# Optimization experiments

Hardware: AMD Instinct MI355X
Metric: run time of the kernel (lower is better)

The kernel has to match this reference:

```python
import jax, jax.numpy as jnp
import numpy as np
from jax import lax

B, T, H, E, V, ENC = 2048, 48, 512, 256, 128, 1024


def setup_inputs() -> dict:
    key = jax.random.key(0)
    ks = jax.random.split(key, 13)
    s = 0.05  # weight scale to keep activations sane
    return {
        "tgt_ids": jax.random.randint(ks[0], (B, T), 0, V),
        "enc_hid": jax.random.normal(ks[1], (B, ENC), jnp.float32),
        "W_init1": s * jax.random.normal(ks[2], (ENC, H), jnp.float32),
        "W_init2": s * jax.random.normal(ks[3], (ENC, H), jnp.float32),
        "embed_table": s * jax.random.normal(ks[4], (V, E), jnp.float32),
        "k1": s * jax.random.normal(ks[5], (E, 3 * H), jnp.float32),
        "rk1": s * jax.random.normal(ks[6], (H, 3 * H), jnp.float32),
        "b1": jnp.zeros((2, 3 * H), jnp.float32),
        "k2": s * jax.random.normal(ks[7], (H, 3 * H), jnp.float32),
        "rk2": s * jax.random.normal(ks[8], (H, 3 * H), jnp.float32),
        "b2": jnp.zeros((2, 3 * H), jnp.float32),
        "Wv": s * jax.random.normal(ks[9], (H, V), jnp.float32),
        "bv": jnp.zeros((V,), jnp.float32),
    }


def gru_masked(x_proj, mask, h0, rk, rb):
    """Keras GRU (reset_after=True, gate order z,r,h) with mask carry-through.
    x_proj: [B,T,3H] precomputed x@kernel + input_bias. mask: [B,T] bool.
    Masked steps keep previous state AND previous output (Keras masking semantics;
    GRU output == state)."""
    def step(h, inp):
        xg, m = inp  # xg: [B,3H], m: [B]
        inner = h @ rk + rb  # [B,3H]
        xz, xr, xh = jnp.split(xg, 3, axis=-1)
        rz, rr, rh = jnp.split(inner, 3, axis=-1)
        z = jax.nn.sigmoid(xz + rz)
        r = jax.nn.sigmoid(xr + rr)
        hh = jnp.tanh(xh + r * rh)
        h_new = z * h + (1.0 - z) * hh
        h = jnp.where(m[:, None], h_new, h)
        return h, h

    _, seq = lax.scan(step, h0, (x_proj.transpose(1, 0, 2), mask.T))
    return seq.transpose(1, 0, 2)  # [B,T,H]


def reference(tgt_ids, enc_hid, W_init1, W_init2, embed_table,
              k1, rk1, b1, k2, rk2, b2, Wv, bv):
    mask = tgt_ids != 0  # mask_zero=True
    emb = embed_table[tgt_ids]  # [B,T,E]
    h01 = enc_hid @ W_init1  # Dense no-bias init of layer-1 state
    h02 = enc_hid @ W_init2
    x1 = emb @ k1 + b1[0]  # [B,T,3H]
    seq1 = gru_masked(x1, mask, h01, rk1, b1[1])
    x2 = seq1 @ k2 + b2[0]
    seq2 = gru_masked(x2, mask, h02, rk2, b2[1])
    probs = jax.nn.softmax(seq2 @ Wv + bv, axis=-1)  # [B,T,V]
    return probs
```

## Files before the change

kernel.cpp:

```cpp
#include <hip/hip_runtime.h>
#include <hip/hip_bf16.h>
#include <math.h>

#define B_   2048
#define T_   48
#define H_   512
#define E_   256
#define V_   128
#define ENC_ 1024
#define H3_  1536
#define BH_  (B_ * H_)
#define NBLK_ 512

typedef __attribute__((ext_vector_type(8))) short bf16x8;
typedef __attribute__((ext_vector_type(4))) float f32x4;
typedef unsigned short ushort_t;

#if defined(__has_builtin)
#if __has_builtin(__builtin_amdgcn_global_load_lds)
#define HAVE_ASYNC 1
#endif
#endif
#ifndef HAVE_ASYNC
#define HAVE_ASYNC 0
#endif

__device__ __forceinline__ void stage16(const ushort_t* g, ushort_t* l, int lane)
{
#if HAVE_ASYNC
    __builtin_amdgcn_global_load_lds(
        (const __attribute__((address_space(1))) unsigned int*)g,
        (__attribute__((address_space(3))) unsigned int*)l, 16, 0, 0);
#else
    *(bf16x8*)(l + lane * 8) = *(const bf16x8*)g;
#endif
}

__device__ __forceinline__ float sigmoidf_(float x) { return 1.0f / (1.0f + expf(-x)); }

__device__ __forceinline__ void tile_map(int lin, int& m0, int& i0)
{
    i0 = ((((lin & 7) << 1) | ((lin >> 3) & 1))) * 32;
    m0 = (lin >> 4) * 64;
}

constexpr int BM = 64, BN = 64, BK = 16;

__global__ __launch_bounds__(256) void gemm_f32(
    const float* __restrict__ A, const float* __restrict__ Bm,
    const float* __restrict__ bias, float* __restrict__ C,
    int M, int N, int K)
{
    __shared__ float As[BK][BM + 4];
    __shared__ float Bs[BK][BN + 4];

    const int tid = threadIdx.x;
    const int bm = blockIdx.y * BM;
    const int bn = blockIdx.x * BN;
    const int tm = (tid >> 4) * 4;
    const int tn = (tid & 15) * 4;
    const int lmA = tid >> 2;
    const int lkA = (tid & 3) * 4;
    const int lkB = tid >> 4;
    const int lnB = (tid & 15) * 4;

    float acc[4][4] = {};

    for (int k0 = 0; k0 < K; k0 += BK) {
        float4 av  = *(const float4*)(A  + (size_t)(bm + lmA) * K + (k0 + lkA));
        float4 bv4 = *(const float4*)(Bm + (size_t)(k0 + lkB) * N + (bn + lnB));
        As[lkA + 0][lmA] = av.x;
        As[lkA + 1][lmA] = av.y;
        As[lkA + 2][lmA] = av.z;
        As[lkA + 3][lmA] = av.w;
        *(float4*)&Bs[lkB][lnB] = bv4;
        __syncthreads();

        #pragma unroll
        for (int k = 0; k < BK; ++k) {
            float4 a = *(const float4*)&As[k][tm];
            float4 b = *(const float4*)&Bs[k][tn];
            acc[0][0] += a.x * b.x; acc[0][1] += a.x * b.y; acc[0][2] += a.x * b.z; acc[0][3] += a.x * b.w;
            acc[1][0] += a.y * b.x; acc[1][1] += a.y * b.y; acc[1][2] += a.y * b.z; acc[1][3] += a.y * b.w;
            acc[2][0] += a.z * b.x; acc[2][1] += a.z * b.y; acc[2][2] += a.z * b.z; acc[2][3] += a.z * b.w;
            acc[3][0] += a.w * b.x; acc[3][1] += a.w * b.y; acc[3][2] += a.w * b.z; acc[3][3] += a.w * b.w;
        }
        __syncthreads();
    }

    #pragma unroll
    for (int r = 0; r < 4; ++r)
        #pragma unroll
        for (int c = 0; c < 4; ++c) {
            float v = acc[r][c];
            if (bias) v += bias[bn + tn + c];
            C[(size_t)(bm + tm + r) * N + (bn + tn + c)] = v;
        }
}

__global__ __launch_bounds__(256) void transpose_to_bf16(
    const float* __restrict__ W, __hip_bfloat16* __restrict__ Wt, int K, int N)
{
    __shared__ float tile[32][33];
    const int bk = blockIdx.y * 32, bn = blockIdx.x * 32;
    const int tx = threadIdx.x & 31, ty = threadIdx.x >> 5;
    #pragma unroll
    for (int i = ty; i < 32; i += 8)
        tile[i][tx] = W[(size_t)(bk + i) * N + (bn + tx)];
    __syncthreads();
    #pragma unroll
    for (int i = ty; i < 32; i += 8)
        Wt[(size_t)(bn + i) * K + (bk + tx)] = __float2bfloat16(tile[tx][i]);
}

__global__ __launch_bounds__(256) void transpose_split(
    const float* __restrict__ W, __hip_bfloat16* __restrict__ Whi,
    __hip_bfloat16* __restrict__ Wlo, int K, int N)
{
    __shared__ float tile[32][33];
    const int bk = blockIdx.y * 32, bn = blockIdx.x * 32;
    const int tx = threadIdx.x & 31, ty = threadIdx.x >> 5;
    #pragma unroll
    for (int i = ty; i < 32; i += 8)
        tile[i][tx] = W[(size_t)(bk + i) * N + (bn + tx)];
    __syncthreads();
    #pragma unroll
    for (int i = ty; i < 32; i += 8) {
        const float v = tile[tx][i];
        const __hip_bfloat16 h = __float2bfloat16(v);
        Whi[(size_t)(bn + i) * K + (bk + tx)] = h;
        Wlo[(size_t)(bn + i) * K + (bk + tx)] = __float2bfloat16(v - __bfloat162float(h));
    }
}

__global__ __launch_bounds__(256) void split_cast(
    const float* __restrict__ x, __hip_bfloat16* __restrict__ hi,
    __hip_bfloat16* __restrict__ lo, int n)
{
    const int i0 = (blockIdx.x * 256 + threadIdx.x) * 4;
    if (i0 >= n) return;
    const float4 v = *(const float4*)(x + i0);
    const float vv[4] = { v.x, v.y, v.z, v.w };
    #pragma unroll
    for (int j = 0; j < 4; ++j) {
        const __hip_bfloat16 h = __float2bfloat16(vv[j]);
        hi[i0 + j] = h;
        lo[i0 + j] = __float2bfloat16(vv[j] - __bfloat162float(h));
    }
}

__global__ __launch_bounds__(256, 2) void init_mfma(
    const ushort_t* __restrict__ ehi, const ushort_t* __restrict__ elo,
    const ushort_t* __restrict__ w1hi, const ushort_t* __restrict__ w1lo,
    const ushort_t* __restrict__ w2hi, const ushort_t* __restrict__ w2lo,
    float* __restrict__ h1f, __hip_bfloat16* __restrict__ h1b,
    float* __restrict__ h2f, __hip_bfloat16* __restrict__ h2b)
{
    const ushort_t* whi = blockIdx.z ? w2hi : w1hi;
    const ushort_t* wlo = blockIdx.z ? w2lo : w1lo;
    float* hf = blockIdx.z ? h2f : h1f;
    __hip_bfloat16* hb = blockIdx.z ? h2b : h1b;

    __shared__ __attribute__((aligned(16))) ushort_t Ahi[2][4096];
    __shared__ __attribute__((aligned(16))) ushort_t Alo[2][4096];
    __shared__ __attribute__((aligned(16))) ushort_t Bhi[2][2048];
    __shared__ __attribute__((aligned(16))) ushort_t Blo[2][2048];

    const int tid  = threadIdx.x;
    const int lane = tid & 63;
    const int w    = tid >> 6;
    const int ln   = lane & 15;
    const int kg   = lane >> 4;
    const int wr   = w >> 1, wc = w & 1;
    const int m0   = blockIdx.y * 64;
    const int i0   = blockIdx.x * 32;

    const int crow = lane >> 3;
    const int ckof = ((lane & 7) ^ crow) * 8;
    const int ko0 = (kg * 8) ^ ((ln & 7) * 8);
    const int ko1 = (32 + kg * 8) ^ ((ln & 7) * 8);

    auto STG = [&](int pb, int k0) {
        #pragma unroll
        for (int c = w; c < 24; c += 4) {
            const ushort_t* g; ushort_t* l;
            if (c < 8) {
                g = ehi + (size_t)(m0 + c * 8 + crow) * ENC_ + k0 + ckof;
                l = &Ahi[pb][c * 512];
            } else if (c < 16) {
                const int cc = c - 8;
                g = elo + (size_t)(m0 + cc * 8 + crow) * ENC_ + k0 + ckof;
                l = &Alo[pb][cc * 512];
            } else if (c < 20) {
                const int cc = c - 16;
                g = whi + (size_t)(i0 + cc * 8 + crow) * ENC_ + k0 + ckof;
                l = &Bhi[pb][cc * 512];
            } else {
                const int cc = c - 20;
                g = wlo + (size_t)(i0 + cc * 8 + crow) * ENC_ + k0 + ckof;
                l = &Blo[pb][cc * 512];
            }
            stage16(g, l, lane);
        }
    };

    f32x4 acc[2] = {};
    STG(0, 0);
    __syncthreads();
    int buf = 0;
    for (int k0 = 0; k0 < ENC_; k0 += 64) {
        if (k0 + 64 < ENC_) STG(buf ^ 1, k0 + 64);
        #pragma unroll
        for (int kk = 0; kk < 2; ++kk) {
            const int ko = kk ? ko1 : ko0;
            bf16x8 ah[2], al[2], bh, bl;
            #pragma unroll
            for (int fm = 0; fm < 2; ++fm) {
                ah[fm] = *(const bf16x8*)(&Ahi[buf][(wr * 32 + fm * 16 + ln) * 64 + ko]);
                al[fm] = *(const bf16x8*)(&Alo[buf][(wr * 32 + fm * 16 + ln) * 64 + ko]);
            }
            bh = *(const bf16x8*)(&Bhi[buf][(wc * 16 + ln) * 64 + ko]);
            bl = *(const bf16x8*)(&Blo[buf][(wc * 16 + ln) * 64 + ko]);
            #pragma unroll
            for (int fm = 0; fm < 2; ++fm) {
                acc[fm] = __builtin_amdgcn_mfma_f32_16x16x32_bf16(ah[fm], bh, acc[fm], 0, 0, 0);
                acc[fm] = __builtin_amdgcn_mfma_f32_16x16x32_bf16(al[fm], bh, acc[fm], 0, 0, 0);
                acc[fm] = __builtin_amdgcn_mfma_f32_16x16x32_bf16(ah[fm], bl, acc[fm], 0, 0, 0);
            }
        }
        __syncthreads();
        buf ^= 1;
    }

    const int i = i0 + wc * 16 + ln;
    #pragma unroll
    for (int fm = 0; fm < 2; ++fm)
        #pragma unroll
        for (int r = 0; r < 4; ++r) {
            const int b = m0 + wr * 32 + fm * 16 + kg * 4 + r;
            const float v = acc[fm][r];
            hf[(size_t)b * H_ + i] = v;
            hb[(size_t)b * H_ + i] = __float2bfloat16(v);
        }
}

__device__ __forceinline__ void l1_phase(
    ushort_t* Al0, ushort_t* Bl0,
    int m0, int i0, int i, int t,
    const int* __restrict__ tgt, const float* __restrict__ xe1,
    const ushort_t* __restrict__ rkt,
    float rbz, float rbr, float rbh,
    const ushort_t* __restrict__ hb_cur,
    __hip_bfloat16* __restrict__ hb_nxt,
    float (&hv)[2][4])
{
    const int tid  = threadIdx.x;
    const int lane = tid & 63;
    const int w    = tid >> 6;
    const int ln   = lane & 15;
    const int kg   = lane >> 4;
    const int wr   = w >> 1, wc = w & 1;
    (void)wc;

    const int crow = lane >> 3;
    const int ckof = ((lane & 7) ^ crow) * 8;

    int ids[2][4];
    #pragma unroll
    for (int fm = 0; fm < 2; ++fm)
        #pragma unroll
        for (int r = 0; r < 4; ++r) {
            const int b = m0 + wr * 32 + fm * 16 + kg * 4 + r;
            ids[fm][r] = tgt[(size_t)b * T_ + t];
        }
    float xgz[2][4], xgr[2][4], xgh[2][4];
    #pragma unroll
    for (int fm = 0; fm < 2; ++fm)
        #pragma unroll
        for (int r = 0; r < 4; ++r) {
            const float* xg = xe1 + (size_t)ids[fm][r] * H3_;
            xgz[fm][r] = xg[i]; xgr[fm][r] = xg[H_ + i]; xgh[fm][r] = xg[2 * H_ + i];
        }

    const int ko0 = (kg * 8) ^ ((ln & 7) * 8);
    const int ko1 = (32 + kg * 8) ^ ((ln & 7) * 8);

    f32x4 acc[2][3] = {};

    auto STAGE = [&](int pb, int k0) {
        #pragma unroll
        for (int c = w; c < 20; c += 4) {
            const ushort_t* g; ushort_t* l;
            if (c < 8) {
                g = hb_cur + (size_t)(m0 + c * 8 + crow) * H_ + k0 + ckof;
                l = Al0 + pb * 4096 + c * 512;
            } else {
                const int idx = c - 8;
                g = rkt + (size_t)((idx >> 2) * H_ + i0 + (idx & 3) * 8 + crow) * H_ + k0 + ckof;
                l = Bl0 + pb * 6144 + idx * 512;
            }
            stage16(g, l, lane);
        }
    };

    STAGE(0, 0);
    __syncthreads();
    int buf = 0;
    for (int k0 = 0; k0 < H_; k0 += 64) {
        if (k0 + 64 < H_) STAGE(buf ^ 1, k0 + 64);
        #pragma unroll
        for (int kk = 0; kk < 2; ++kk) {
            const int ko = kk ? ko1 : ko0;
            bf16x8 af[2], bf[3];
            #pragma unroll
            for (int fm = 0; fm < 2; ++fm)
                af[fm] = *(const bf16x8*)(Al0 + buf * 4096 + (wr * 32 + fm * 16 + ln) * 64 + ko);
            #pragma unroll
            for (int g = 0; g < 3; ++g)
                bf[g] = *(const bf16x8*)(Bl0 + buf * 6144 + g * 2048 + ((w & 1) * 16 + ln) * 64 + ko);
            #pragma unroll
            for (int fm = 0; fm < 2; ++fm)
                #pragma unroll
                for (int g = 0; g < 3; ++g)
                    acc[fm][g] = __builtin_amdgcn_mfma_f32_16x16x32_bf16(
                        af[fm], bf[g], acc[fm][g], 0, 0, 0);
        }
        __syncthreads();
        buf ^= 1;
    }

    #pragma unroll
    for (int fm = 0; fm < 2; ++fm)
        #pragma unroll
        for (int r = 0; r < 4; ++r) {
            const int b = m0 + wr * 32 + fm * 16 + kg * 4 + r;
            const float hvv = hv[fm][r];
            float z  = sigmoidf_(xgz[fm][r] + acc[fm][0][r] + rbz);
            float rr = sigmoidf_(xgr[fm][r] + acc[fm][1][r] + rbr);
            float hh = tanhf(xgh[fm][r] + rr * (acc[fm][2][r] + rbh));
            float hn = (ids[fm][r] != 0) ? (z * hvv + (1.0f - z) * hh) : hvv;
            hv[fm][r] = hn;
            hb_nxt[(size_t)b * H_ + i] = __float2bfloat16(hn);
        }
}

__device__ __forceinline__ void l2_phase(
    ushort_t* lds,
    int m0, int i0, int i, int t,
    const int* __restrict__ tgt,
    const ushort_t* __restrict__ k2t, const ushort_t* __restrict__ rk2t,
    float bxz, float bxr, float bxh,
    float brz, float brr, float brh,
    const ushort_t* __restrict__ s1b,
    const ushort_t* __restrict__ a1, size_t a1s,
    __hip_bfloat16* __restrict__ hbo, size_t hos,
    float (&hv)[2][4])
{
    ushort_t* A0l = lds;
    ushort_t* A1l = lds + 8192;
    ushort_t* B0l = lds + 16384;
    ushort_t* B1l = lds + 22528;

    const int tid  = threadIdx.x;
    const int lane = tid & 63;
    const int w    = tid >> 6;
    const int ln   = lane & 15;
    const int kg   = lane >> 4;
    const int wr   = w >> 1, wc = w & 1;
    (void)wc;

    const int crow = lane >> 3;
    const int ckof = ((lane & 7) ^ crow) * 8;

    int ids[2][4];
    #pragma unroll
    for (int fm = 0; fm < 2; ++fm)
        #pragma unroll
        for (int r = 0; r < 4; ++r) {
            const int b = m0 + wr * 32 + fm * 16 + kg * 4 + r;
            ids[fm][r] = tgt[(size_t)b * T_ + t];
        }

    const int ko0 = (kg * 8) ^ ((ln & 7) * 8);
    const int ko1 = (32 + kg * 8) ^ ((ln & 7) * 8);

    auto STAGE_A = [&](int pb, int k0) {
        #pragma unroll
        for (int c = w; c < 16; c += 4) {
            const ushort_t* g; ushort_t* l;
            if (c < 8) {
                g = s1b + (size_t)(m0 + c * 8 + crow) * H_ + k0 + ckof;
                l = A0l + pb * 4096 + c * 512;
            } else {
                const int cc = c - 8;
                g = a1 + (size_t)(m0 + cc * 8 + crow) * a1s + k0 + ckof;
                l = A1l + pb * 4096 + cc * 512;
            }
            stage16(g, l, lane);
        }
    };
    auto STAGE_B = [&](int k0) {
        #pragma unroll
        for (int c = w; c < 24; c += 4) {
            const ushort_t* g; ushort_t* l;
            if (c < 12) {
                g = k2t + (size_t)((c >> 2) * H_ + i0 + (c & 3) * 8 + crow) * H_ + k0 + ckof;
                l = B0l + c * 512;
            } else {
                const int idx = c - 12;
                g = rk2t + (size_t)((idx >> 2) * H_ + i0 + (idx & 3) * 8 + crow) * H_ + k0 + ckof;
                l = B1l + idx * 512;
            }
            stage16(g, l, lane);
        }
    };

    f32x4 acc0[2][3] = {};
    f32x4 acc1[2][3] = {};

    STAGE_A(0, 0);
    STAGE_B(0);
    __syncthreads();
    int buf = 0;
    for (int k0 = 0; k0 < H_; k0 += 64) {
        const bool more = (k0 + 64 < H_);
        if (more) STAGE_A(buf ^ 1, k0 + 64);

        bf16x8 a0f[2][2], a1f[2][2], b0f[2][3], b1f[2][3];
        #pragma unroll
        for (int kk = 0; kk < 2; ++kk) {
            const int ko = kk ? ko1 : ko0;
            #pragma unroll
            for (int fm = 0; fm < 2; ++fm) {
                a0f[kk][fm] = *(const bf16x8*)(A0l + buf * 4096 + (wr * 32 + fm * 16 + ln) * 64 + ko);
                a1f[kk][fm] = *(const bf16x8*)(A1l + buf * 4096 + (wr * 32 + fm * 16 + ln) * 64 + ko);
            }
            #pragma unroll
            for (int g = 0; g < 3; ++g) {
                b0f[kk][g] = *(const bf16x8*)(B0l + g * 2048 + ((w & 1) * 16 + ln) * 64 + ko);
                b1f[kk][g] = *(const bf16x8*)(B1l + g * 2048 + ((w & 1) * 16 + ln) * 64 + ko);
            }
        }
        __builtin_amdgcn_sched_barrier(0);
        asm volatile("s_waitcnt lgkmcnt(0)" ::: "memory");
        __builtin_amdgcn_sched_barrier(0);
        __builtin_amdgcn_s_barrier();
        if (more) STAGE_B(k0 + 64);

        #pragma unroll
        for (int kk = 0; kk < 2; ++kk)
            #pragma unroll
            for (int fm = 0; fm < 2; ++fm)
                #pragma unroll
                for (int g = 0; g < 3; ++g) {
                    acc0[fm][g] = __builtin_amdgcn_mfma_f32_16x16x32_bf16(
                        a0f[kk][fm], b0f[kk][g], acc0[fm][g], 0, 0, 0);
                    acc1[fm][g] = __builtin_amdgcn_mfma_f32_16x16x32_bf16(
                        a1f[kk][fm], b1f[kk][g], acc1[fm][g], 0, 0, 0);
                }
        __syncthreads();
        buf ^= 1;
    }

    #pragma unroll
    for (int fm = 0; fm < 2; ++fm)
        #pragma unroll
        for (int r = 0; r < 4; ++r) {
            const int b = m0 + wr * 32 + fm * 16 + kg * 4 + r;
            const float hvv = hv[fm][r];
            float z  = sigmoidf_((acc0[fm][0][r] + bxz) + (acc1[fm][0][r] + brz));
            float rr = sigmoidf_((acc0[fm][1][r] + bxr) + (acc1[fm][1][r] + brr));
            float hh = tanhf((acc0[fm][2][r] + bxh) + rr * (acc1[fm][2][r] + brh));
            float hn = (ids[fm][r] != 0) ? (z * hvv + (1.0f - z) * hh) : hvv;
            hv[fm][r] = hn;
            hbo[(size_t)b * hos + i] = __float2bfloat16(hn);
        }
}

__global__ __launch_bounds__(256, 2) void l1_fused(
    const int* __restrict__ tgt, int t,
    const float* __restrict__ xe1, const ushort_t* __restrict__ rkt,
    const float* __restrict__ rb,
    const float* __restrict__ hf_cur, const ushort_t* __restrict__ hb_cur,
    float* __restrict__ hf_nxt, __hip_bfloat16* __restrict__ hb_nxt)
{
    __shared__ __attribute__((aligned(16))) ushort_t lds[20480];
    int m0, i0; tile_map(blockIdx.x, m0, i0);
    const int tid = threadIdx.x, lane = tid & 63, w = tid >> 6;
    const int ln = lane & 15, kg = lane >> 4, wr = w >> 1, wc = w & 1;
    const int i = i0 + wc * 16 + ln;

    float hv[2][4];
    #pragma unroll
    for (int fm = 0; fm < 2; ++fm)
        #pragma unroll
        for (int r = 0; r < 4; ++r)
            hv[fm][r] = hf_cur[(size_t)(m0 + wr * 32 + fm * 16 + kg * 4 + r) * H_ + i];

    l1_phase(lds, lds + 8192, m0, i0, i, t, tgt, xe1, rkt,
             rb[i], rb[H_ + i], rb[2 * H_ + i], hb_cur, hb_nxt, hv);

    #pragma unroll
    for (int fm = 0; fm < 2; ++fm)
        #pragma unroll
        for (int r = 0; r < 4; ++r)
            hf_nxt[(size_t)(m0 + wr * 32 + fm * 16 + kg * 4 + r) * H_ + i] = hv[fm][r];
}

__global__ __launch_bounds__(256, 2) void l2_fused(
    const int* __restrict__ tgt, int t,
    const ushort_t* __restrict__ k2t, const ushort_t* __restrict__ rk2t,
    const float* __restrict__ bx, const float* __restrict__ br,
    const ushort_t* __restrict__ s1b,
    const float* __restrict__ hf_cur,
    const ushort_t* __restrict__ hb_cur, size_t hbs,
    float* __restrict__ hf_nxt,
    __hip_bfloat16* __restrict__ hbo, size_t hos)
{
    __shared__ __attribute__((aligned(16))) ushort_t lds[28672];
    int m0, i0; tile_map(blockIdx.x, m0, i0);
    const int tid = threadIdx.x, lane = tid & 63, w = tid >> 6;
    const int ln = lane & 15, kg = lane >> 4, wr = w >> 1, wc = w & 1;
    const int i = i0 + wc * 16 + ln;

    float hv[2][4];
    #pragma unroll
    for (int fm = 0; fm < 2; ++fm)
        #pragma unroll
        for (int r = 0; r < 4; ++r)
            hv[fm][r] = hf_cur[(size_t)(m0 + wr * 32 + fm * 16 + kg * 4 + r) * H_ + i];

    l2_phase(lds, m0, i0, i, t, tgt, k2t, rk2t,
             bx[i], bx[H_ + i], bx[2 * H_ + i],
             br[i], br[H_ + i], br[2 * H_ + i],
             s1b, hb_cur, hbs, hbo, hos, hv);

    #pragma unroll
    for (int fm = 0; fm < 2; ++fm)
        #pragma unroll
        for (int r = 0; r < 4; ++r)
            hf_nxt[(size_t)(m0 + wr * 32 + fm * 16 + kg * 4 + r) * H_ + i] = hv[fm][r];
}

__device__ __forceinline__ void grid_barrier(unsigned* bar)
{
    __syncthreads();
    if (threadIdx.x == 0) {
        __threadfence();
        const unsigned g = __hip_atomic_load(&bar[1], __ATOMIC_RELAXED, __HIP_MEMORY_SCOPE_AGENT);
        const unsigned arrived =
            __hip_atomic_fetch_add(&bar[0], 1u, __ATOMIC_ACQ_REL, __HIP_MEMORY_SCOPE_AGENT) + 1u;
        if (arrived == (unsigned)NBLK_) {
            __hip_atomic_store(&bar[0], 0u, __ATOMIC_RELAXED, __HIP_MEMORY_SCOPE_AGENT);
            __hip_atomic_store(&bar[1], g + 1u, __ATOMIC_RELEASE, __HIP_MEMORY_SCOPE_AGENT);
        } else {
            while (__hip_atomic_load(&bar[1], __ATOMIC_ACQUIRE, __HIP_MEMORY_SCOPE_AGENT) == g)
                __builtin_amdgcn_s_sleep(2);
        }
        __threadfence();
    }
    __syncthreads();
}

__global__ __launch_bounds__(256, 2) void recurrence_all(
    const int* __restrict__ tgt, const float* __restrict__ xe1,
    const ushort_t* __restrict__ rk1t, const float* __restrict__ rb1,
    const ushort_t* __restrict__ k2t, const ushort_t* __restrict__ rk2t,
    const float* __restrict__ bx, const float* __restrict__ br,
    const float* __restrict__ h1f0, __hip_bfloat16* __restrict__ h1b,
    const float* __restrict__ h2f0, const __hip_bfloat16* __restrict__ h2b0,
    __hip_bfloat16* __restrict__ seq2b, unsigned* __restrict__ bar)
{
    __shared__ __attribute__((aligned(16))) ushort_t lds[28672];
    int m0, i0; tile_map(blockIdx.x, m0, i0);
    const int tid = threadIdx.x, lane = tid & 63, w = tid >> 6;
    const int ln = lane & 15, kg = lane >> 4, wr = w >> 1, wc = w & 1;
    const int i = i0 + wc * 16 + ln;

    const float rbz = rb1[i], rbr = rb1[H_ + i], rbh = rb1[2 * H_ + i];
    const float bxz = bx[i],  bxr = bx[H_ + i],  bxh = bx[2 * H_ + i];
    const float brz = br[i],  brr = br[H_ + i],  brh = br[2 * H_ + i];

    float hv1[2][4], hv2[2][4];
    #pragma unroll
    for (int fm = 0; fm < 2; ++fm)
        #pragma unroll
        for (int r = 0; r < 4; ++r) {
            const size_t b = (size_t)(m0 + wr * 32 + fm * 16 + kg * 4 + r) * H_ + i;
            hv1[fm][r] = h1f0[b];
            hv2[fm][r] = h2f0[b];
        }

    l1_phase(lds, lds + 8192, m0, i0, i, 0, tgt, xe1, rk1t, rbz, rbr, rbh,
             (const ushort_t*)h1b, h1b + BH_, hv1);
    grid_barrier(bar);

    #pragma unroll 1
    for (int p = 0; p < T_; ++p) {
        const ushort_t* a1 = (p == 0)
            ? (const ushort_t*)h2b0
            : (const ushort_t*)(seq2b + (size_t)(p - 1) * H_);
        const size_t a1s = (p == 0) ? (size_t)H_ : (size_t)T_ * H_;
        const ushort_t* s1 = (const ushort_t*)(h1b + (size_t)((p + 1) & 1) * BH_);

        l2_phase(lds, m0, i0, i, p, tgt, k2t, rk2t,
                 bxz, bxr, bxh, brz, brr, brh,
                 s1, a1, a1s,
                 seq2b + (size_t)p * H_, (size_t)T_ * H_, hv2);

        if (p + 1 < T_)
            l1_phase(lds, lds + 8192, m0, i0, i, p + 1, tgt, xe1, rk1t,
                     rbz, rbr, rbh,
                     (const ushort_t*)(h1b + (size_t)((p + 1) & 1) * BH_),
                     h1b + (size_t)((p + 2) & 1) * BH_, hv1);

        grid_barrier(bar);
    }
}

__device__ __forceinline__ void softmax_write4(
    float ax, float ay, float az, float aw, float* __restrict__ outp, int cg)
{
    float m = fmaxf(fmaxf(ax, ay), fmaxf(az, aw));
    #pragma unroll
    for (int d = 16; d >= 1; d >>= 1) m = fmaxf(m, __shfl_xor(m, d));
    float ex = __expf(ax - m), ey = __expf(ay - m),
          ez = __expf(az - m), ew = __expf(aw - m);
    float s = ex + ey + ez + ew;
    #pragma unroll
    for (int d = 16; d >= 1; d >>= 1) s += __shfl_xor(s, d);
    float inv = 1.0f / s;
    float4 o; o.x = ex * inv; o.y = ey * inv; o.z = ez * inv; o.w = ew * inv;
    *(float4*)(outp + cg * 4) = o;
}

__global__ __launch_bounds__(256) void out_softmax(
    const float* __restrict__ h2, const float* __restrict__ Wv,
    const float* __restrict__ bv, float* __restrict__ out, int t)
{
    const int tid = threadIdx.x;
    const int cg = tid & 31;
    const int rg = tid >> 5;
    const int row0 = blockIdx.x * 16;

    __shared__ float hs[16][512];
    for (int idx = tid; idx < 16 * 512; idx += 256)
        hs[idx >> 9][idx & 511] = h2[(size_t)(row0 + (idx >> 9)) * 512 + (idx & 511)];
    __syncthreads();

    const int r0 = rg * 2;
    const float4 bvv = *(const float4*)(bv + cg * 4);
    float a0x = bvv.x, a0y = bvv.y, a0z = bvv.z, a0w = bvv.w;
    float a1x = bvv.x, a1y = bvv.y, a1z = bvv.z, a1w = bvv.w;

    #pragma unroll 4
    for (int k = 0; k < 512; ++k) {
        float4 wv = *(const float4*)(Wv + (size_t)k * V_ + cg * 4);
        float h0 = hs[r0][k], h1 = hs[r0 + 1][k];
        a0x += h0 * wv.x; a0y += h0 * wv.y; a0z += h0 * wv.z; a0w += h0 * wv.w;
        a1x += h1 * wv.x; a1y += h1 * wv.y; a1z += h1 * wv.z; a1w += h1 * wv.w;
    }

    softmax_write4(a0x, a0y, a0z, a0w, out + ((size_t)(row0 + r0) * T_ + t) * V_, cg);
    softmax_write4(a1x, a1y, a1z, a1w, out + ((size_t)(row0 + r0 + 1) * T_ + t) * V_, cg);
}

__global__ __launch_bounds__(256) void proj_mfma(
    const ushort_t* __restrict__ s2, const ushort_t* __restrict__ wvt,
    const float* __restrict__ bv, float* __restrict__ out)
{
    const int lane = threadIdx.x & 63;
    const int w    = threadIdx.x >> 6;
    const int ln   = lane & 15;
    const int kg   = lane >> 4;
    const size_t row0 = (size_t)blockIdx.x * 128 + (size_t)w * 32;

    float bvl[8];
    #pragma unroll
    for (int nf = 0; nf < 8; ++nf) bvl[nf] = bv[nf * 16 + ln];

    f32x4 acc[2][8] = {};
    #pragma unroll 2
    for (int k0 = 0; k0 < H_; k0 += 32) {
        bf16x8 af[2], bf[8];
        #pragma unroll
        for (int mf = 0; mf < 2; ++mf)
            af[mf] = *(const bf16x8*)(s2 + (row0 + mf * 16 + ln) * H_ + k0 + kg * 8);
        #pragma unroll
        for (int nf = 0; nf < 8; ++nf)
            bf[nf] = *(const bf16x8*)(wvt + (size_t)(nf * 16 + ln) * H_ + k0 + kg * 8);
        #pragma unroll
        for (int mf = 0; mf < 2; ++mf)
            #pragma unroll
            for (int nf = 0; nf < 8; ++nf)
                acc[mf][nf] = __builtin_amdgcn_mfma_f32_16x16x32_bf16(
                    af[mf], bf[nf], acc[mf][nf], 0, 0, 0);
    }

    #pragma unroll
    for (int mf = 0; mf < 2; ++mf)
        #pragma unroll
        for (int q = 0; q < 4; ++q) {
            float v[8];
            float m = -1e30f;
            #pragma unroll
            for (int nf = 0; nf < 8; ++nf) { v[nf] = acc[mf][nf][q] + bvl[nf]; m = fmaxf(m, v[nf]); }
            #pragma unroll
            for (int d = 1; d <= 8; d <<= 1) m = fmaxf(m, __shfl_xor(m, d));
            float s = 0.f;
            #pragma unroll
            for (int nf = 0; nf < 8; ++nf) { v[nf] = __expf(v[nf] - m); s += v[nf]; }
            #pragma unroll
            for (int d = 1; d <= 8; d <<= 1) s += __shfl_xor(s, d);
            const float inv = 1.0f / s;
            float* op = out + (row0 + mf * 16 + kg * 4 + q) * V_;
            #pragma unroll
            for (int nf = 0; nf < 8; ++nf) op[nf * 16 + ln] = v[nf] * inv;
        }
}

extern "C" void kernel_launch(void* const* d_in, const int* in_sizes, int n_in,
                              void* d_out, int out_size, void* d_ws, size_t ws_size,
                              hipStream_t stream)
{
    const int*   tgt  = (const int*)  d_in[0];
    const float* enc  = (const float*)d_in[1];
    const float* Wi1  = (const float*)d_in[2];
    const float* Wi2  = (const float*)d_in[3];
    const float* emb  = (const float*)d_in[4];
    const float* k1   = (const float*)d_in[5];
    const float* rk1  = (const float*)d_in[6];
    const float* b1   = (const float*)d_in[7];
    const float* k2   = (const float*)d_in[8];
    const float* rk2  = (const float*)d_in[9];
    const float* b2   = (const float*)d_in[10];
    const float* Wv   = (const float*)d_in[11];
    const float* bv   = (const float*)d_in[12];
    float* out = (float*)d_out;

    float* ws  = (float*)d_ws;
    float* xe1 = ws;
    float* h1f = xe1 + (size_t)V_ * H3_;
    float* h2f = h1f + (size_t)2 * BH_;
    __hip_bfloat16* h1b = (__hip_bfloat16*)(h2f + (size_t)2 * BH_);
    __hip_bfloat16* h2b = h1b + (size_t)2 * BH_;
    __hip_bfloat16* rk1t = h2b + (size_t)2 * BH_;
    __hip_bfloat16* k2t  = rk1t + (size_t)H3_ * H_;
    __hip_bfloat16* rk2t = k2t  + (size_t)H3_ * H_;
    __hip_bfloat16* wvt  = rk2t + (size_t)H3_ * H_;
    __hip_bfloat16* ehi  = wvt + (size_t)V_ * H_;
    __hip_bfloat16* elo  = ehi + (size_t)B_ * ENC_;
    __hip_bfloat16* w1hi = elo + (size_t)B_ * ENC_;
    __hip_bfloat16* w1lo = w1hi + (size_t)H_ * ENC_;
    __hip_bfloat16* w2hi = w1lo + (size_t)H_ * ENC_;
    __hip_bfloat16* w2lo = w2hi + (size_t)H_ * ENC_;
    __hip_bfloat16* seq2b = w2lo + (size_t)H_ * ENC_;
    unsigned* bar = (unsigned*)(seq2b + (size_t)B_ * T_ * H_);

    const size_t need = (size_t)((char*)bar + 64 - (char*)d_ws);
    const bool batched = ws_size >= need;

    static int persist_state = -1;
    if (persist_state < 0) {
        int nb = 0;
        hipError_t e1 = hipOccupancyMaxActiveBlocksPerMultiprocessor(&nb, recurrence_all, 256, 0);
        hipDeviceProp_t prop;
        hipError_t e2 = hipGetDeviceProperties(&prop, 0);
        persist_state = (e1 == hipSuccess && e2 == hipSuccess &&
                         (long)nb * prop.multiProcessorCount >= NBLK_) ? 1 : 0;
// ... 74 lines not shown
```

Measured before the change: 1.529 ms.

## Fuse layer-1 and layer-2 GRU steps into one shared K-loop per timestep

Merges the separate layer-1 and layer-2 recurrence phases into one templated routine. Both layers' GEMMs now share one K loop over the h1 tile, which is staged once and used for both rk1 and k2. This removes a separate staging pass, its sync points and a second pipeline prologue per timestep, at the cost of more LDS (34816 shorts) and more accumulator registers, which may lower occupancy. The grid barrier is also changed to a monotonic phase counter with explicit release/acquire fences and no counter reset.

```diff
diff --git a/kernel.cpp b/kernel.cpp
--- a/kernel.cpp
+++ b/kernel.cpp
@@ -244,179 +244,108 @@
         }
 }
 
-__device__ __forceinline__ void l1_phase(
-    ushort_t* Al0, ushort_t* Bl0,
-    int m0, int i0, int i, int t,
+template<int MODE>
+__device__ __forceinline__ void fused_phase(
+    ushort_t* lds, int m0, int i0, int i, int t1, int t2,
     const int* __restrict__ tgt, const float* __restrict__ xe1,
-    const ushort_t* __restrict__ rkt,
+    const ushort_t* __restrict__ rk1t,
     float rbz, float rbr, float rbh,
-    const ushort_t* __restrict__ hb_cur,
-    __hip_bfloat16* __restrict__ hb_nxt,
-    float (&hv)[2][4])
-{
-    const int tid  = threadIdx.x;
-    const int lane = tid & 63;
-    const int w    = tid >> 6;
-    const int ln   = lane & 15;
-    const int kg   = lane >> 4;
-    const int wr   = w >> 1, wc = w & 1;
-    (void)wc;
-
+    const ushort_t* __restrict__ k2t, const ushort_t* __restrict__ rk2t,
+    float bxz, float bxr, float bxh, float brz, float brr, float brh,
+    const ushort_t* __restrict__ h1cur,
+    const ushort_t* __restrict__ h2cur, size_t h2s,
+    __hip_bfloat16* __restrict__ h1nxt,
+    __hip_bfloat16* __restrict__ sout, size_t souts,
+    float (&hv1)[2][4], float (&hv2)[2][4])
+{
+    ushort_t* A1l = lds;
+    ushort_t* A2l = lds + 8192;
+    ushort_t* B1l = lds + 16384;
+    ushort_t* B2l = lds + 22528;
+    ushort_t* B3l = lds + 28672;
+
+    const int tid = threadIdx.x, lane = tid & 63, w = tid >> 6;
+    const int ln = lane & 15, kg = lane >> 4, wr = w >> 1;
     const int crow = lane >> 3;
     const int ckof = ((lane & 7) ^ crow) * 8;
-
-    int ids[2][4];
+    const int ko0 = (kg * 8) ^ ((ln & 7) * 8);
+    const int ko1 = (32 + kg * 8) ^ ((ln & 7) * 8);
+
+    int ids1[2][4], ids2[2][4];
+    float xgz[2][4], xgr[2][4], xgh[2][4];
     #pragma unroll
     for (int fm = 0; fm < 2; ++fm)
         #pragma unroll
         for (int r = 0; r < 4; ++r) {
             const int b = m0 + wr * 32 + fm * 16 + kg * 4 + r;
-            ids[fm][r] = tgt[(size_t)b * T_ + t];
-        }
-    float xgz[2][4], xgr[2][4], xgh[2][4];
-    #pragma unroll
-    for (int fm = 0; fm < 2; ++fm)
-        #pragma unroll
-        for (int r = 0; r < 4; ++r) {
-            const float* xg = xe1 + (size_t)ids[fm][r] * H3_;
-            xgz[fm][r] = xg[i]; xgr[fm][r] = xg[H_ + i]; xgh[fm][r] = xg[2 * H_ + i];
-        }
-
-    const int ko0 = (kg * 8) ^ ((ln & 7) * 8);
-    const int ko1 = (32 + kg * 8) ^ ((ln & 7) * 8);
-
-    f32x4 acc[2][3] = {};
-
-    auto STAGE = [&](int pb, int k0) {
-        #pragma unroll
-        for (int c = w; c < 20; c += 4) {
+            if (MODE != 2) ids1[fm][r] = tgt[(size_t)b * T_ + t1];
+            if (MODE != 1) ids2[fm][r] = tgt[(size_t)b * T_ + t2];
+        }
+    if (MODE != 2) {
+        #pragma unroll
+        for (int fm = 0; fm < 2; ++fm)
+            #pragma unroll
+            for (int r = 0; r < 4; ++r) {
+                const float* xg = xe1 + (size_t)ids1[fm][r] * H3_;
+                xgz[fm][r] = xg[i]; xgr[fm][r] = xg[H_ + i]; xgh[fm][r] = xg[2 * H_ + i];
+            }
+    }
+
+    constexpr int NA = (MODE == 1) ? 8 : 16;
+    constexpr int NB = (MODE == 0) ? 36 : ((MODE == 1) ? 12 : 24);
+
+    auto STAGE_A = [&](int pb, int k0) {
+        #pragma unroll
+        for (int c = w; c < NA; c += 4) {
             const ushort_t* g; ushort_t* l;
             if (c < 8) {
-                g = hb_cur + (size_t)(m0 + c * 8 + crow) * H_ + k0 + ckof;
-                l = Al0 + pb * 4096 + c * 512;
-            } else {
-                const int idx = c - 8;
-                g = rkt + (size_t)((idx >> 2) * H_ + i0 + (idx & 3) * 8 + crow) * H_ + k0 + ckof;
-                l = Bl0 + pb * 6144 + idx * 512;
-            }
-            stage16(g, l, lane);
-        }
-    };
-
-    STAGE(0, 0);
-    __syncthreads();
-    int buf = 0;
-    for (int k0 = 0; k0 < H_; k0 += 64) {
-        if (k0 + 64 < H_) STAGE(buf ^ 1, k0 + 64);
-        #pragma unroll
-        for (int kk = 0; kk < 2; ++kk) {
-            const int ko = kk ? ko1 : ko0;
-            bf16x8 af[2], bf[3];
-            #pragma unroll
-            for (int fm = 0; fm < 2; ++fm)
-                af[fm] = *(const bf16x8*)(Al0 + buf * 4096 + (wr * 32 + fm * 16 + ln) * 64 + ko);
-            #pragma unroll
-            for (int g = 0; g < 3; ++g)
-                bf[g] = *(const bf16x8*)(Bl0 + buf * 6144 + g * 2048 + ((w & 1) * 16 + ln) * 64 + ko);
-            #pragma unroll
-            for (int fm = 0; fm < 2; ++fm)
-                #pragma unroll
-                for (int g = 0; g < 3; ++g)
-                    acc[fm][g] = __builtin_amdgcn_mfma_f32_16x16x32_bf16(
-                        af[fm], bf[g], acc[fm][g], 0, 0, 0);
-        }
-        __syncthreads();
-        buf ^= 1;
-    }
-
-    #pragma unroll
-    for (int fm = 0; fm < 2; ++fm)
-        #pragma unroll
-        for (int r = 0; r < 4; ++r) {
-            const int b = m0 + wr * 32 + fm * 16 + kg * 4 + r;
-            const float hvv = hv[fm][r];
-            float z  = sigmoidf_(xgz[fm][r] + acc[fm][0][r] + rbz);
-            float rr = sigmoidf_(xgr[fm][r] + acc[fm][1][r] + rbr);
-            float hh = tanhf(xgh[fm][r] + rr * (acc[fm][2][r] + rbh));
-            float hn = (ids[fm][r] != 0) ? (z * hvv + (1.0f - z) * hh) : hvv;
-            hv[fm][r] = hn;
-            hb_nxt[(size_t)b * H_ + i] = __float2bfloat16(hn);
-        }
-}
-
-__device__ __forceinline__ void l2_phase(
-    ushort_t* lds,
-    int m0, int i0, int i, int t,
-    const int* __restrict__ tgt,
-    const ushort_t* __restrict__ k2t, const ushort_t* __restrict__ rk2t,
-    float bxz, float bxr, float bxh,
-    float brz, float brr, float brh,
-    const ushort_t* __restrict__ s1b,
-    const ushort_t* __restrict__ a1, size_t a1s,
-    __hip_bfloat16* __restrict__ hbo, size_t hos,
-    float (&hv)[2][4])
-{
-    ushort_t* A0l = lds;
-    ushort_t* A1l = lds + 8192;
-    ushort_t* B0l = lds + 16384;
-    ushort_t* B1l = lds + 22528;
-
-    const int tid  = threadIdx.x;
-    const int lane = tid & 63;
-    const int w    = tid >> 6;
-    const int ln   = lane & 15;
-    const int kg   = lane >> 4;
-    const int wr   = w >> 1, wc = w & 1;
-    (void)wc;
-
-    const int crow = lane >> 3;
-    const int ckof = ((lane & 7) ^ crow) * 8;
-
-    int ids[2][4];
-    #pragma unroll
-    for (int fm = 0; fm < 2; ++fm)
-        #pragma unroll
-        for (int r = 0; r < 4; ++r) {
-            const int b = m0 + wr * 32 + fm * 16 + kg * 4 + r;
-            ids[fm][r] = tgt[(size_t)b * T_ + t];
-        }
-
-    const int ko0 = (kg * 8) ^ ((ln & 7) * 8);
-    const int ko1 = (32 + kg * 8) ^ ((ln & 7) * 8);
-
-    auto STAGE_A = [&](int pb, int k0) {
-        #pragma unroll
-        for (int c = w; c < 16; c += 4) {
-            const ushort_t* g; ushort_t* l;
-            if (c < 8) {
-                g = s1b + (size_t)(m0 + c * 8 + crow) * H_ + k0 + ckof;
-                l = A0l + pb * 4096 + c * 512;
+                g = h1cur + (size_t)(m0 + c * 8 + crow) * H_ + k0 + ckof;
+                l = A1l + pb * 4096 + c * 512;
             } else {
                 const int cc = c - 8;
-                g = a1 + (size_t)(m0 + cc * 8 + crow) * a1s + k0 + ckof;
-                l = A1l + pb * 4096 + cc * 512;
+                g = h2cur + (size_t)(m0 + cc * 8 + crow) * h2s + k0 + ckof;
+                l = A2l + pb * 4096 + cc * 512;
             }
             stage16(g, l, lane);
         }
     };
     auto STAGE_B = [&](int k0) {
         #pragma unroll
-        for (int c = w; c < 24; c += 4) {
+        for (int c = w; c < NB; c += 4) {
             const ushort_t* g; ushort_t* l;
-            if (c < 12) {
-                g = k2t + (size_t)((c >> 2) * H_ + i0 + (c & 3) * 8 + crow) * H_ + k0 + ckof;
-                l = B0l + c * 512;
+            if (MODE == 1) {
+                g = rk1t + (size_t)((c >> 2) * H_ + i0 + (c & 3) * 8 + crow) * H_ + k0 + ckof;
+                l = B1l + c * 512;
+            } else if (MODE == 2) {
+                if (c < 12) {
+                    g = k2t + (size_t)((c >> 2) * H_ + i0 + (c & 3) * 8 + crow) * H_ + k0 + ckof;
+                    l = B2l + c * 512;
+                } else {
+                    const int d = c - 12;
+                    g = rk2t + (size_t)((d >> 2) * H_ + i0 + (d & 3) * 8 + crow) * H_ + k0 + ckof;
+                    l = B3l + d * 512;
+                }
             } else {
-                const int idx = c - 12;
-                g = rk2t + (size_t)((idx >> 2) * H_ + i0 + (idx & 3) * 8 + crow) * H_ + k0 + ckof;
-                l = B1l + idx * 512;
+                if (c < 12) {
+                    g = rk1t + (size_t)((c >> 2) * H_ + i0 + (c & 3) * 8 + crow) * H_ + k0 + ckof;
+                    l = B1l + c * 512;
+                } else if (c < 24) {
+                    const int d = c - 12;
+                    g = k2t + (size_t)((d >> 2) * H_ + i0 + (d & 3) * 8 + crow) * H_ + k0 + ckof;
+                    l = B2l + d * 512;
+                } else {
+                    const int d = c - 24;
+                    g = rk2t + (size_t)((d >> 2) * H_ + i0 + (d & 3) * 8 + crow) * H_ + k0 + ckof;
+                    l = B3l + d * 512;
+                }
             }
             stage16(g, l, lane);
         }
     };
 
-    f32x4 acc0[2][3] = {};
     f32x4 acc1[2][3] = {};
+    f32x4 accx[2][3] = {};
+    f32x4 accr[2][3] = {};
 
     STAGE_A(0, 0);
     STAGE_B(0);
@@ -426,19 +355,24 @@
         const bool more = (k0 + 64 < H_);
         if (more) STAGE_A(buf ^ 1, k0 + 64);
 
-        bf16x8 a0f[2][2], a1f[2][2], b0f[2][3], b1f[2][3];
+        bf16x8 a1f[2][2], a2f[2][2], b1f[2][3], b2f[2][3], b3f[2][3];
         #pragma unroll
         for (int kk = 0; kk < 2; ++kk) {
             const int ko = kk ? ko1 : ko0;
             #pragma unroll
             for (int fm = 0; fm < 2; ++fm) {
-                a0f[kk][fm] = *(const bf16x8*)(A0l + buf * 4096 + (wr * 32 + fm * 16 + ln) * 64 + ko);
                 a1f[kk][fm] = *(const bf16x8*)(A1l + buf * 4096 + (wr * 32 + fm * 16 + ln) * 64 + ko);
+                if (MODE != 1)
+                    a2f[kk][fm] = *(const bf16x8*)(A2l + buf * 4096 + (wr * 32 + fm * 16 + ln) * 64 + ko);
             }
             #pragma unroll
             for (int g = 0; g < 3; ++g) {
-                b0f[kk][g] = *(const bf16x8*)(B0l + g * 2048 + ((w & 1) * 16 + ln) * 64 + ko);
-                b1f[kk][g] = *(const bf16x8*)(B1l + g * 2048 + ((w & 1) * 16 + ln) * 64 + ko);
+                if (MODE != 2)
+                    b1f[kk][g] = *(const bf16x8*)(B1l + g * 2048 + ((w & 1) * 16 + ln) * 64 + ko);
+                if (MODE != 1) {
+                    b2f[kk][g] = *(const bf16x8*)(B2l + g * 2048 + ((w & 1) * 16 + ln) * 64 + ko);
+                    b3f[kk][g] = *(const bf16x8*)(B3l + g * 2048 + ((w & 1) * 16 + ln) * 64 + ko);
+                }
             }
         }
         __builtin_amdgcn_sched_barrier(0);
@@ -453,28 +387,50 @@
             for (int fm = 0; fm < 2; ++fm)
                 #pragma unroll
                 for (int g = 0; g < 3; ++g) {
-                    acc0[fm][g] = __builtin_amdgcn_mfma_f32_16x16x32_bf16(
-                        a0f[kk][fm], b0f[kk][g], acc0[fm][g], 0, 0, 0);
-                    acc1[fm][g] = __builtin_amdgcn_mfma_f32_16x16x32_bf16(
-                        a1f[kk][fm], b1f[kk][g], acc1[fm][g], 0, 0, 0);
+                    if (MODE != 2)
+                        acc1[fm][g] = __builtin_amdgcn_mfma_f32_16x16x32_bf16(
+                            a1f[kk][fm], b1f[kk][g], acc1[fm][g], 0, 0, 0);
+                    if (MODE != 1) {
+                        accx[fm][g] = __builtin_amdgcn_mfma_f32_16x16x32_bf16(
+                            a1f[kk][fm], b2f[kk][g], accx[fm][g], 0, 0, 0);
+                        accr[fm][g] = __builtin_amdgcn_mfma_f32_16x16x32_bf16(
+                            a2f[kk][fm], b3f[kk][g], accr[fm][g], 0, 0, 0);
+                    }
                 }
         __syncthreads();
         buf ^= 1;
     }
 
-    #pragma unroll
-    for (int fm = 0; fm < 2; ++fm)
-        #pragma unroll
-        for (int r = 0; r < 4; ++r) {
-            const int b = m0 + wr * 32 + fm * 16 + kg * 4 + r;
-            const float hvv = hv[fm][r];
-            float z  = sigmoidf_((acc0[fm][0][r] + bxz) + (acc1[fm][0][r] + brz));
-            float rr = sigmoidf_((acc0[fm][1][r] + bxr) + (acc1[fm][1][r] + brr));
-            float hh = tanhf((acc0[fm][2][r] + bxh) + rr * (acc1[fm][2][r] + brh));
-            float hn = (ids[fm][r] != 0) ? (z * hvv + (1.0f - z) * hh) : hvv;
-            hv[fm][r] = hn;
-            hbo[(size_t)b * hos + i] = __float2bfloat16(hn);
-        }
+    if (MODE != 2) {
+        #pragma unroll
+        for (int fm = 0; fm < 2; ++fm)
+            #pragma unroll
+            for (int r = 0; r < 4; ++r) {
+                const int b = m0 + wr * 32 + fm * 16 + kg * 4 + r;
+                const float hvv = hv1[fm][r];
+                float z  = sigmoidf_(xgz[fm][r] + acc1[fm][0][r] + rbz);
+                float rr = sigmoidf_(xgr[fm][r] + acc1[fm][1][r] + rbr);
+                float hh = tanhf(xgh[fm][r] + rr * (acc1[fm][2][r] + rbh));
+                float hn = (ids1[fm][r] != 0) ? (z * hvv + (1.0f - z) * hh) : hvv;
+                hv1[fm][r] = hn;
+                h1nxt[(size_t)b * H_ + i] = __float2bfloat16(hn);
+            }
+    }
+    if (MODE != 1) {
+        #pragma unroll
+        for (int fm = 0; fm < 2; ++fm)
+            #pragma unroll
+            for (int r = 0; r < 4; ++r) {
+                const int b = m0 + wr * 32 + fm * 16 + kg * 4 + r;
+                const float hvv = hv2[fm][r];
+                float z  = sigmoidf_((accx[fm][0][r] + bxz) + (accr[fm][0][r] + brz));
+                float rr = sigmoidf_((accx[fm][1][r] + bxr) + (accr[fm][1][r] + brr));
+                float hh = tanhf((accx[fm][2][r] + bxh) + rr * (accr[fm][2][r] + brh));
+                float hn = (ids2[fm][r] != 0) ? (z * hvv + (1.0f - z) * hh) : hvv;
+                hv2[fm][r] = hn;
+                sout[(size_t)b * souts + i] = __float2bfloat16(hn);
+            }
+    }
 }
 
 __global__ __launch_bounds__(256, 2) void l1_fused(
@@ -484,27 +440,29 @@
     const float* __restrict__ hf_cur, const ushort_t* __restrict__ hb_cur,
     float* __restrict__ hf_nxt, __hip_bfloat16* __restrict__ hb_nxt)
 {
-    __shared__ __attribute__((aligned(16))) ushort_t lds[20480];
+    __shared__ __attribute__((aligned(16))) ushort_t lds[34816];
     int m0, i0; tile_map(blockIdx.x, m0, i0);
     const int tid = threadIdx.x, lane = tid & 63, w = tid >> 6;
     const int ln = lane & 15, kg = lane >> 4, wr = w >> 1, wc = w & 1;
     const int i = i0 + wc * 16 + ln;
 
-    float hv[2][4];
+    float hv1[2][4], hv2[2][4];
     #pragma unroll
     for (int fm = 0; fm < 2; ++fm)
         #pragma unroll
         for (int r = 0; r < 4; ++r)
-            hv[fm][r] = hf_cur[(size_t)(m0 + wr * 32 + fm * 16 + kg * 4 + r) * H_ + i];
-
-    l1_phase(lds, lds + 8192, m0, i0, i, t, tgt, xe1, rkt,
-             rb[i], rb[H_ + i], rb[2 * H_ + i], hb_cur, hb_nxt, hv);
+            hv1[fm][r] = hf_cur[(size_t)(m0 + wr * 32 + fm * 16 + kg * 4 + r) * H_ + i];
+
+    fused_phase<1>(lds, m0, i0, i, t, 0, tgt, xe1, rkt,
+                   rb[i], rb[H_ + i], rb[2 * H_ + i],
+                   nullptr, nullptr, 0.f, 0.f, 0.f, 0.f, 0.f, 0.f,
+                   hb_cur, nullptr, 0, hb_nxt, nullptr, 0, hv1, hv2);
 
     #pragma unroll
     for (int fm = 0; fm < 2; ++fm)
         #pragma unroll
         for (int r = 0; r < 4; ++r)
-            hf_nxt[(size_t)(m0 + wr * 32 + fm * 16 + kg * 4 + r) * H_ + i] = hv[fm][r];
+            hf_nxt[(size_t)(m0 + wr * 32 + fm * 16 + kg * 4 + r) * H_ + i] = hv1[fm][r];
 }
 
 __global__ __launch_bounds__(256, 2) void l2_fused(
@@ -517,47 +475,47 @@
     float* __restrict__ hf_nxt,
     __hip_bfloat16* __restrict__ hbo, size_t hos)
 {
-    __shared__ __attribute__((aligned(16))) ushort_t lds[28672];
+    __shared__ __attribute__((aligned(16))) ushort_t lds[34816];
     int m0, i0; tile_map(blockIdx.x, m0, i0);
     const int tid = threadIdx.x, lane = tid & 63, w = tid >> 6;
     const int ln = lane & 15, kg = lane >> 4, wr = w >> 1, wc = w & 1;
     const int i = i0 + wc * 16 + ln;
 
-    float hv[2][4];
+    float hv1[2][4], hv2[2][4];
     #pragma unroll
     for (int fm = 0; fm < 2; ++fm)
         #pragma unroll
         for (int r = 0; r < 4; ++r)
-            hv[fm][r] = hf_cur[(size_t)(m0 + wr * 32 + fm * 16 + kg * 4 + r) * H_ + i];
-
-    l2_phase(lds, m0, i0, i, t, tgt, k2t, rk2t,
-             bx[i], bx[H_ + i], bx[2 * H_ + i],
-             br[i], br[H_ + i], br[2 * H_ + i],
-             s1b, hb_cur, hbs, hbo, hos, hv);
+            hv2[fm][r] = hf_cur[(size_t)(m0 + wr * 32 + fm * 16 + kg * 4 + r) * H_ + i];
+
+    fused_phase<2>(lds, m0, i0, i, 0, t, tgt, nullptr, nullptr,
+                   0.f, 0.f, 0.f,
+                   k2t, rk2t,
+                   bx[i], bx[H_ + i], bx[2 * H_ + i],
+                   br[i], br[H_ + i], br[2 * H_ + i],
+                   s1b, hb_cur, hbs, nullptr, hbo, hos, hv1, hv2);
 
     #pragma unroll
     for (int fm = 0; fm < 2; ++fm)
         #pragma unroll
         for (int r = 0; r < 4; ++r)
-            hf_nxt[(size_t)(m0 + wr * 32 + fm * 16 + kg * 4 + r) * H_ + i] = hv[fm][r];
-}
-
-__device__ __forceinline__ void grid_barrier(unsigned* bar)
+            hf_nxt[(size_t)(m0 + wr * 32 + fm * 16 + kg * 4 + r) * H_ + i] = hv2[fm][r];
+}
+
+__device__ __forceinline__ void grid_barrier(unsigned* bar, unsigned phase)
 {
     __syncthreads();
     if (threadIdx.x == 0) {
-        __threadfence();
-        const unsigned g = __hip_atomic_load(&bar[1], __ATOMIC_RELAXED, __HIP_MEMORY_SCOPE_AGENT);
+        __builtin_amdgcn_fence(__ATOMIC_RELEASE, "agent");
         const unsigned arrived =
-            __hip_atomic_fetch_add(&bar[0], 1u, __ATOMIC_ACQ_REL, __HIP_MEMORY_SCOPE_AGENT) + 1u;
-        if (arrived == (unsigned)NBLK_) {
-            __hip_atomic_store(&bar[0], 0u, __ATOMIC_RELAXED, __HIP_MEMORY_SCOPE_AGENT);
-            __hip_atomic_store(&bar[1], g + 1u, __ATOMIC_RELEASE, __HIP_MEMORY_SCOPE_AGENT);
+            __hip_atomic_fetch_add(&bar[0], 1u, __ATOMIC_RELAXED, __HIP_MEMORY_SCOPE_AGENT) + 1u;
+        if (arrived == (unsigned)NBLK_ * (phase + 1u)) {
+            __hip_atomic_store(&bar[1], phase + 1u, __ATOMIC_RELAXED, __HIP_MEMORY_SCOPE_AGENT);
         } else {
-            while (__hip_atomic_load(&bar[1], __ATOMIC_ACQUIRE, __HIP_MEMORY_SCOPE_AGENT) == g)
-                __builtin_amdgcn_s_sleep(2);
-        }
-        __threadfence();
+            while (__hip_atomic_load(&bar[1], __ATOMIC_RELAXED, __HIP_MEMORY_SCOPE_AGENT) < phase + 1u)
+                __builtin_amdgcn_s_sleep(4);
+        }
+        __builtin_amdgcn_fence(__ATOMIC_ACQUIRE, "agent");
     }
     __syncthreads();
 }
@@ -571,7 +529,7 @@
     const float* __restrict__ h2f0, const __hip_bfloat16* __restrict__ h2b0,
     __hip_bfloat16* __restrict__ seq2b, unsigned* __restrict__ bar)
 {
-    __shared__ __attribute__((aligned(16))) ushort_t lds[28672];
+    __shared__ __attribute__((aligned(16))) ushort_t lds[34816];
     int m0, i0; tile_map(blockIdx.x, m0, i0);
     const int tid = threadIdx.x, lane = tid & 63, w = tid >> 6;
     const int ln = lane & 15, kg = lane >> 4, wr = w >> 1, wc = w & 1;
@@ -591,30 +549,39 @@
             hv2[fm][r] = h2f0[b];
         }
 
-    l1_phase(lds, lds + 8192, m0, i0, i, 0, tgt, xe1, rk1t, rbz, rbr, rbh,
-             (const ushort_t*)h1b, h1b + BH_, hv1);
-    grid_barrier(bar);
+    unsigned ph = 0;
+
+    fused_phase<1>(lds, m0, i0, i, 0, 0, tgt, xe1, rk1t, rbz, rbr, rbh,
+                   nullptr, nullptr, 0.f, 0.f, 0.f, 0.f, 0.f, 0.f,
+                   (const ushort_t*)h1b, nullptr, 0, h1b + BH_, nullptr, 0,
+                   hv1, hv2);
+    grid_barrier(bar, ph); ++ph;
 
     #pragma unroll 1
-    for (int p = 0; p < T_; ++p) {
-        const ushort_t* a1 = (p == 0)
-            ? (const ushort_t*)h2b0
-            : (const ushort_t*)(seq2b + (size_t)(p - 1) * H_);
-        const size_t a1s = (p == 0) ? (size_t)H_ : (size_t)T_ * H_;
+    for (int p = 0; p < T_ - 1; ++p) {
         const ushort_t* s1 = (const ushort_t*)(h1b + (size_t)((p + 1) & 1) * BH_);
-
-        l2_phase(lds, m0, i0, i, p, tgt, k2t, rk2t,
-                 bxz, bxr, bxh, brz, brr, brh,
-                 s1, a1, a1s,
-                 seq2b + (size_t)p * H_, (size_t)T_ * H_, hv2);
-
-        if (p + 1 < T_)
-            l1_phase(lds, lds + 8192, m0, i0, i, p + 1, tgt, xe1, rk1t,
-                     rbz, rbr, rbh,
-                     (const ushort_t*)(h1b + (size_t)((p + 1) & 1) * BH_),
-                     h1b + (size_t)((p + 2) & 1) * BH_, hv1);
-
-        grid_barrier(bar);
+        const ushort_t* a2 = (p == 0) ? (const ushort_t*)h2b0
+                                      : (const ushort_t*)(seq2b + (size_t)(p - 1) * H_);
+        const size_t a2s = (p == 0) ? (size_t)H_ : (size_t)T_ * H_;
+
+        fused_phase<0>(lds, m0, i0, i, p + 1, p, tgt, xe1, rk1t, rbz, rbr, rbh,
+                       k2t, rk2t, bxz, bxr, bxh, brz, brr, brh,
+                       s1, a2, a2s,
+                       h1b + (size_t)(p & 1) * BH_,
+                       seq2b + (size_t)p * H_, (size_t)T_ * H_,
+                       hv1, hv2);
+        grid_barrier(bar, ph); ++ph;
+    }
+
+    {
+        const int p = T_ - 1;
+        const ushort_t* s1 = (const ushort_t*)(h1b + (size_t)((p + 1) & 1) * BH_);
+        const ushort_t* a2 = (const ushort_t*)(seq2b + (size_t)(p - 1) * H_);
+        fused_phase<2>(lds, m0, i0, i, 0, p, tgt, nullptr, nullptr, 0.f, 0.f, 0.f,
+                       k2t, rk2t, bxz, bxr, bxh, brz, brr, brh,
+                       s1, a2, (size_t)T_ * H_,
+                       nullptr, seq2b + (size_t)p * H_, (size_t)T_ * H_,
+                       hv1, hv2);
     }
 }
 
```

Measured after the change: 1.548 ms. About the same (+1.2%).

## Unpipeline the layer schedule and use a monotonic-counter grid barrier

Applied to the files above, without the earlier changes.

Drops the skewed schedule, where layer-2 step p and layer-1 step p+1 shared one barrier interval. Each timestep now runs layer 1, a grid barrier, then layer 2 and another barrier. The grid barrier becomes a monotonic phase counter with relaxed atomics plus explicit release/acquire fences, with no reset store. The block-to-tile mapping is re-swizzled. Roughly twice as many grid barriers per sequence trade away the cross-layer overlap. The counter also depends on the barrier memory being zeroed before every launch.

```diff
diff --git a/kernel.cpp b/kernel.cpp
--- a/kernel.cpp
+++ b/kernel.cpp
@@ -40,8 +40,9 @@
 
 __device__ __forceinline__ void tile_map(int lin, int& m0, int& i0)
 {
-    i0 = ((((lin & 7) << 1) | ((lin >> 3) & 1))) * 32;
-    m0 = (lin >> 4) * 64;
+    const int swz = (lin & 7) * 64 + (lin >> 3);
+    m0 = (swz >> 4) * 64;
+    i0 = (swz & 15) * 32;
 }
 
 constexpr int BM = 64, BN = 64, BK = 16;
@@ -259,8 +260,7 @@
     const int w    = tid >> 6;
     const int ln   = lane & 15;
     const int kg   = lane >> 4;
-    const int wr   = w >> 1, wc = w & 1;
-    (void)wc;
+    const int wr   = w >> 1;
 
     const int crow = lane >> 3;
     const int ckof = ((lane & 7) ^ crow) * 8;
@@ -366,8 +366,7 @@
     const int w    = tid >> 6;
     const int ln   = lane & 15;
     const int kg   = lane >> 4;
-    const int wr   = w >> 1, wc = w & 1;
-    (void)wc;
+    const int wr   = w >> 1;
 
     const int crow = lane >> 3;
     const int ckof = ((lane & 7) ^ crow) * 8;
@@ -542,22 +541,20 @@
             hf_nxt[(size_t)(m0 + wr * 32 + fm * 16 + kg * 4 + r) * H_ + i] = hv[fm][r];
 }
 
-__device__ __forceinline__ void grid_barrier(unsigned* bar)
+__device__ __forceinline__ void grid_barrier(unsigned* bar, unsigned phase)
 {
     __syncthreads();
     if (threadIdx.x == 0) {
-        __threadfence();
-        const unsigned g = __hip_atomic_load(&bar[1], __ATOMIC_RELAXED, __HIP_MEMORY_SCOPE_AGENT);
+        __builtin_amdgcn_fence(__ATOMIC_RELEASE, "agent");
         const unsigned arrived =
-            __hip_atomic_fetch_add(&bar[0], 1u, __ATOMIC_ACQ_REL, __HIP_MEMORY_SCOPE_AGENT) + 1u;
-        if (arrived == (unsigned)NBLK_) {
-            __hip_atomic_store(&bar[0], 0u, __ATOMIC_RELAXED, __HIP_MEMORY_SCOPE_AGENT);
-            __hip_atomic_store(&bar[1], g + 1u, __ATOMIC_RELEASE, __HIP_MEMORY_SCOPE_AGENT);
+            __hip_atomic_fetch_add(&bar[0], 1u, __ATOMIC_RELAXED, __HIP_MEMORY_SCOPE_AGENT) + 1u;
+        if (arrived == (unsigned)NBLK_ * (phase + 1u)) {
+            __hip_atomic_store(&bar[1], phase + 1u, __ATOMIC_RELAXED, __HIP_MEMORY_SCOPE_AGENT);
         } else {
-            while (__hip_atomic_load(&bar[1], __ATOMIC_ACQUIRE, __HIP_MEMORY_SCOPE_AGENT) == g)
-                __builtin_amdgcn_s_sleep(2);
-        }
-        __threadfence();
+            while (__hip_atomic_load(&bar[1], __ATOMIC_RELAXED, __HIP_MEMORY_SCOPE_AGENT) < phase + 1u)
+                __builtin_amdgcn_s_sleep(4);
+        }
+        __builtin_amdgcn_fence(__ATOMIC_ACQUIRE, "agent");
     }
     __syncthreads();
 }
@@ -591,30 +588,29 @@
             hv2[fm][r] = h2f0[b];
         }
 
-    l1_phase(lds, lds + 8192, m0, i0, i, 0, tgt, xe1, rk1t, rbz, rbr, rbh,
-             (const ushort_t*)h1b, h1b + BH_, hv1);
-    grid_barrier(bar);
+    unsigned ph = 0;
 
     #pragma unroll 1
-    for (int p = 0; p < T_; ++p) {
-        const ushort_t* a1 = (p == 0)
+    for (int t = 0; t < T_; ++t) {
+        const int cur = t & 1, nxt = cur ^ 1;
+
+        l1_phase(lds, lds + 8192, m0, i0, i, t, tgt, xe1, rk1t,
+                 rbz, rbr, rbh,
+                 (const ushort_t*)(h1b + (size_t)cur * BH_),
+                 h1b + (size_t)nxt * BH_, hv1);
+        grid_barrier(bar, ph); ++ph;
+
+        const ushort_t* a1 = (t == 0)
             ? (const ushort_t*)h2b0
-            : (const ushort_t*)(seq2b + (size_t)(p - 1) * H_);
-        const size_t a1s = (p == 0) ? (size_t)H_ : (size_t)T_ * H_;
-        const ushort_t* s1 = (const ushort_t*)(h1b + (size_t)((p + 1) & 1) * BH_);
-
-        l2_phase(lds, m0, i0, i, p, tgt, k2t, rk2t,
+            : (const ushort_t*)(seq2b + (size_t)(t - 1) * H_);
+        const size_t a1s = (t == 0) ? (size_t)H_ : (size_t)T_ * H_;
+
+        l2_phase(lds, m0, i0, i, t, tgt, k2t, rk2t,
                  bxz, bxr, bxh, brz, brr, brh,
-                 s1, a1, a1s,
-                 seq2b + (size_t)p * H_, (size_t)T_ * H_, hv2);
-
-        if (p + 1 < T_)
-            l1_phase(lds, lds + 8192, m0, i0, i, p + 1, tgt, xe1, rk1t,
-                     rbz, rbr, rbh,
-                     (const ushort_t*)(h1b + (size_t)((p + 1) & 1) * BH_),
-                     h1b + (size_t)((p + 2) & 1) * BH_, hv1);
-
-        grid_barrier(bar);
+                 (const ushort_t*)(h1b + (size_t)nxt * BH_),
+                 a1, a1s,
+                 seq2b + (size_t)t * H_, (size_t)T_ * H_, hv2);
+        if (t + 1 < T_) { grid_barrier(bar, ph); ++ph; }
     }
 }
 
```

After: 1.515 ms. Within noise of the previous version (-1.0%).
